# Kernel optimization log

Hardware: AMD Instinct MI355X
Metric: run time of the kernel (lower is better)

## Reference

```python
import jax, jax.numpy as jnp
import numpy as np

B, S, D = 2, 2048, 1024
H, HD = 16, 64  # num_heads, head_dim; H*HD == D


def setup_inputs() -> dict:
    key = jax.random.key(0)
    ks = jax.random.split(key, 5)
    scale = 1.0 / np.sqrt(D)
    return {
        "inputs": jax.random.normal(ks[0], (B, S, D), jnp.float32),
        "Wq": jax.random.normal(ks[1], (D, H * HD), jnp.float32) * scale,
        "bq": jnp.zeros((H * HD,), jnp.float32),
        "Wk": jax.random.normal(ks[2], (D, H * HD), jnp.float32) * scale,
        "bk": jnp.zeros((H * HD,), jnp.float32),
        "Wv": jax.random.normal(ks[3], (D, H * HD), jnp.float32) * scale,
        "bv": jnp.zeros((H * HD,), jnp.float32),
        "Wo": jax.random.normal(ks[4], (H * HD, D), jnp.float32) * scale,
        "bo": jnp.zeros((D,), jnp.float32),
    }


def reference(inputs, Wq, bq, Wk, bk, Wv, bv, Wo, bo):
    b, s, _ = inputs.shape
    # QKV projections, split into heads: [b, s, H, HD]
    q = (inputs @ Wq + bq).reshape(b, s, H, HD)
    k = (inputs @ Wk + bk).reshape(b, s, H, HD)
    v = (inputs @ Wv + bv).reshape(b, s, H, HD)
    # scaled dot-product attention (non-causal, full)
    scores = jnp.einsum('bqhd,bkhd->bhqk', q, k) / jnp.sqrt(jnp.float32(HD))
    attn = jax.nn.softmax(scores, axis=-1)
    out = jnp.einsum('bhql,blhd->bqhd', attn, v).reshape(b, s, H * HD)
    return out @ Wo + bo
```

## Files before the change

### kernel.cpp

```cpp
#include <hip/hip_runtime.h>
#include <hip/hip_bf16.h>

typedef __attribute__((ext_vector_type(8))) _Float16 half8;
typedef __attribute__((ext_vector_type(4))) _Float16 half4;
typedef __attribute__((ext_vector_type(2))) _Float16 half2v;
typedef __attribute__((ext_vector_type(4))) __fp16 fp16x4;
typedef __attribute__((ext_vector_type(4))) float f32x4;

#define MFMA16(a, b, c) __builtin_amdgcn_mfma_f32_16x16x32_f16(a, b, c, 0, 0, 0)
#define MFMA16K16(a, b, c)                                                         \
    __builtin_amdgcn_mfma_f32_16x16x16f16(__builtin_bit_cast(fp16x4, a),           \
                                          __builtin_bit_cast(fp16x4, b), c, 0, 0, 0)

typedef const __attribute__((address_space(1))) unsigned int GU32;
typedef __attribute__((address_space(3))) unsigned int LU32;

__device__ __forceinline__ void async_copy16(const _Float16* g, _Float16* l) {
    __builtin_amdgcn_global_load_lds((GU32*)g, (LU32*)l, 16, 0, 0);
}

__device__ __forceinline__ half2v pack2(float a, float b) {
    return __builtin_bit_cast(half2v, __builtin_amdgcn_cvt_pkrtz(a, b));
}

#define QSCALE 0.18033688011112042f


__global__ __launch_bounds__(256) void prep(
    const float* __restrict__ X, _Float16* __restrict__ Xh,
    const float* __restrict__ W0, const float* __restrict__ W1,
    const float* __restrict__ W2, const float* __restrict__ W3,
    _Float16* __restrict__ T0, _Float16* __restrict__ T1,
    _Float16* __restrict__ T2, _Float16* __restrict__ T3) {
    __shared__ float t[32][33];
    const int bid = blockIdx.x, tid = threadIdx.x;
    if (bid < 4096) {
        int i = (bid * 256 + tid) * 4;
        float4 v = *(const float4*)(X + i);
        half4 o = {(_Float16)v.x, (_Float16)v.y, (_Float16)v.z, (_Float16)v.w};
        *(half4*)(Xh + i) = o;
    } else {
        const int bid2 = bid - 4096;
        const int z = bid2 >> 10, tt = bid2 & 1023;
        const int bx = tt & 31, by = tt >> 5;
        const int tx = tid & 31, ty = tid >> 5;
        const float* src = z == 0 ? W0 : z == 1 ? W1 : z == 2 ? W2 : W3;
        _Float16* dst    = z == 0 ? T0 : z == 1 ? T1 : z == 2 ? T2 : T3;
        const int x = bx * 32 + tx;
        const int y0 = by * 32;
        for (int i = ty; i < 32; i += 8)
            t[i][tx] = src[(size_t)(y0 + i) * 1024 + x];
        __syncthreads();
        const int nx = y0 + tx;
        const int ny = bx * 32;
        for (int i = ty; i < 32; i += 8)
            dst[(size_t)(ny + i) * 1024 + nx] = (_Float16)t[tx][i];
    }
}

__global__ __launch_bounds__(256) void qkv_gemm(
    const _Float16* __restrict__ Xh,
    const _Float16* __restrict__ WTq, const _Float16* __restrict__ WTk,
    const _Float16* __restrict__ WTv,
    const float* __restrict__ bq, const float* __restrict__ bk,
    const float* __restrict__ bv,
    _Float16* __restrict__ Qo, _Float16* __restrict__ Ko,
    _Float16* __restrict__ Vto) {
    __shared__ __attribute__((aligned(16))) _Float16 Als[128 * 32];
    __shared__ __attribute__((aligned(16))) _Float16 Bls[128 * 32];

    const int wsel = blockIdx.y >> 3;
    const _Float16* WT = wsel == 0 ? WTq : wsel == 1 ? WTk : WTv;
    const float* bias  = wsel == 0 ? bq  : wsel == 1 ? bk  : bv;

    const int tid = threadIdx.x, w = tid >> 6, lane = tid & 63;
    const int quad = lane >> 4, l16 = lane & 15;
    const int wr = (w >> 1) * 64, wc = (w & 1) * 64;
    const int mBase = blockIdx.x * 128, nBase = (blockIdx.y & 7) * 128;
    const _Float16* Ab = Xh + (size_t)mBase * 1024;
    const _Float16* Bb = WT + (size_t)nBase * 1024;

    const int sr0 = tid >> 2,          sc0 = (tid & 3) ^ ((sr0 >> 1) & 3);
    const int sr1 = (256 + tid) >> 2,  sc1 = (tid & 3) ^ ((sr1 >> 1) & 3);

    f32x4 acc[4][4] = {};

    for (int k0 = 0; k0 < 1024; k0 += 32) {
        __syncthreads();
        {
            _Float16* lA0 = Als + (size_t)(tid & 192) * 8;
            _Float16* lB0 = Bls + (size_t)(tid & 192) * 8;
            _Float16* lA1 = Als + (size_t)(256 + (tid & 192)) * 8;
            _Float16* lB1 = Bls + (size_t)(256 + (tid & 192)) * 8;
            async_copy16(Ab + (size_t)sr0 * 1024 + k0 + sc0 * 8, lA0);
            async_copy16(Bb + (size_t)sr0 * 1024 + k0 + sc0 * 8, lB0);
            async_copy16(Ab + (size_t)sr1 * 1024 + k0 + sc1 * 8, lA1);
            async_copy16(Bb + (size_t)sr1 * 1024 + k0 + sc1 * 8, lB1);
        }
        __syncthreads();
        half8 af[4], bfr[4];
#pragma unroll
        for (int i = 0; i < 4; ++i) {
            const int row = wr + i * 16 + l16;
            af[i] = ((const half8*)Als)[row * 4 + (quad ^ ((row >> 1) & 3))];
        }
#pragma unroll
        for (int j = 0; j < 4; ++j) {
            const int row = wc + j * 16 + l16;
            bfr[j] = ((const half8*)Bls)[row * 4 + (quad ^ ((row >> 1) & 3))];
        }
#pragma unroll
        for (int i = 0; i < 4; ++i)
#pragma unroll
            for (int j = 0; j < 4; ++j) acc[i][j] = MFMA16(af[i], bfr[j], acc[i][j]);
    }

    const float scale = (wsel == 0) ? QSCALE : 1.0f;
#pragma unroll
    for (int i = 0; i < 4; ++i) {
        const int row = mBase + wr + i * 16 + quad * 4;
#pragma unroll
        for (int j = 0; j < 4; ++j) {
            const int col = nBase + wc + j * 16 + l16;
            const float bb = bias[col];
            if (wsel == 2) {
                const int hh = col >> 6, hd = col & 63;
                const int bi = row >> 11, s = row & 2047;
                half4 pv;
#pragma unroll
                for (int r = 0; r < 4; ++r) pv[r] = (_Float16)((acc[i][j][r] + bb) * scale);
                *(half4*)(Vto + ((size_t)(bi * 16 + hh) * 64 + hd) * 2048 + s) = pv;
            } else {
                _Float16* dst = (wsel == 0) ? Qo : Ko;
#pragma unroll
                for (int r = 0; r < 4; ++r)
                    dst[(size_t)(row + r) * 1024 + col] =
                        (_Float16)((acc[i][j][r] + bb) * scale);
            }
        }
    }
}

__global__ __launch_bounds__(512) void attn_kernel(
    const _Float16* __restrict__ Q, const _Float16* __restrict__ K,
    const _Float16* __restrict__ Vt, _Float16* __restrict__ O) {
    const int bh = blockIdx.y;
    const int b = bh >> 4, h = bh & 15;
    const int qt = blockIdx.x;
    const int tid = threadIdx.x, w = tid >> 6, lane = tid & 63;
    const int quad = lane >> 4, l16 = lane & 15;
    const int ws2 = w & 3, kstream = w >> 2;

    __shared__ __attribute__((aligned(16))) _Float16 smem[32768];
    _Float16 (*Kls)[2][4096] = (_Float16(*)[2][4096])smem;
    _Float16 (*Vls)[2][4096] = (_Float16(*)[2][4096])(smem + 16384);

    const _Float16* Qb = Q  + (size_t)b * 2048 * 1024 + h * 64;
    const _Float16* Kb = K  + (size_t)b * 2048 * 1024 + h * 64;
    const _Float16* Vb = Vt + (size_t)bh * 64 * 2048;

    const int stid = tid & 255, sgrp = tid >> 8;
    const int u0 = stid, u1 = 256 + stid;
    const int r0 = u0 >> 3, c0 = (u0 & 7) ^ (r0 & 7);
    const int r1 = u1 >> 3, c1 = (u1 & 7) ^ (r1 & 7);
    const int lbase0 = (stid & 192) * 8;
    const int lbase1 = 2048 + (stid & 192) * 8;

    half8 qf[2][2];
#pragma unroll
    for (int g = 0; g < 2; ++g) {
        const int q = qt * 128 + ws2 * 32 + g * 16 + l16;
#pragma unroll
        for (int kc = 0; kc < 2; ++kc)
            qf[g][kc] = *(const half8*)(Qb + (size_t)q * 1024 + kc * 32 + quad * 8);
    }

    f32x4 oacc[2][4] = {};
    float l[2] = {0.f, 0.f};

    {
        const int nb = sgrp * 64;
        _Float16* kd = &Kls[sgrp][0][0];
        _Float16* vd = &Vls[sgrp][0][0];
        async_copy16(Kb + (size_t)(nb + r0) * 1024 + c0 * 8, kd + lbase0);
        async_copy16(Kb + (size_t)(nb + r1) * 1024 + c1 * 8, kd + lbase1);
        async_copy16(Vb + (size_t)r0 * 2048 + nb + c0 * 8, vd + lbase0);
        async_copy16(Vb + (size_t)r1 * 2048 + nb + c1 * 8, vd + lbase1);
    }

    const int sw = l16 & 7;
    for (int it = 0; it < 16; ++it) {
        __syncthreads();
        const _Float16* Kc = &Kls[kstream][it & 1][0];
        const _Float16* Vc = &Vls[kstream][it & 1][0];
        if (it + 1 < 16) {
            const int nb = (2 * (it + 1) + sgrp) * 64;
            _Float16* kd = &Kls[sgrp][(it + 1) & 1][0];
            _Float16* vd = &Vls[sgrp][(it + 1) & 1][0];
            async_copy16(Kb + (size_t)(nb + r0) * 1024 + c0 * 8, kd + lbase0);
            async_copy16(Kb + (size_t)(nb + r1) * 1024 + c1 * 8, kd + lbase1);
            async_copy16(Vb + (size_t)r0 * 2048 + nb + c0 * 8, vd + lbase0);
            async_copy16(Vb + (size_t)r1 * 2048 + nb + c1 * 8, vd + lbase1);
        }
        f32x4 s0[4] = {}, s1[4] = {};
#pragma unroll
        for (int nt = 0; nt < 4; ++nt) {
            const int key = nt * 16 + l16;
            half8 k0 = *(const half8*)(Kc + ((size_t)key * 8 + (quad ^ sw)) * 8);
            half8 k1 = *(const half8*)(Kc + ((size_t)key * 8 + ((4 + quad) ^ sw)) * 8);
            s0[nt] = MFMA16(k0, qf[0][0], s0[nt]);
            s0[nt] = MFMA16(k1, qf[0][1], s0[nt]);
            s1[nt] = MFMA16(k0, qf[1][0], s1[nt]);
            s1[nt] = MFMA16(k1, qf[1][1], s1[nt]);
        }
        half4 pB[2][4];
#pragma unroll
        for (int g = 0; g < 2; ++g) {
            f32x4* s = g ? s1 : s0;
#pragma unroll
            for (int nt = 0; nt < 4; ++nt) {
                float p0 = __builtin_amdgcn_exp2f(s[nt][0]);
                float p1 = __builtin_amdgcn_exp2f(s[nt][1]);
                float p2 = __builtin_amdgcn_exp2f(s[nt][2]);
                float p3 = __builtin_amdgcn_exp2f(s[nt][3]);
                l[g] += (p0 + p1) + (p2 + p3);
                ((half2v*)&pB[g][nt])[0] = pack2(p0, p1);
                ((half2v*)&pB[g][nt])[1] = pack2(p2, p3);
            }
        }
#pragma unroll
        for (int nt = 0; nt < 4; ++nt) {
            const int chunk = (nt << 1) + (quad >> 1);
#pragma unroll
            for (int j = 0; j < 4; ++j) {
                const int hd = j * 16 + l16;
                half4 vf = *(const half4*)(Vc + ((size_t)hd * 8 + (chunk ^ sw)) * 8 +
                                           (quad & 1) * 4);
                oacc[0][j] = MFMA16K16(vf, pB[0][nt], oacc[0][j]);
                oacc[1][j] = MFMA16K16(vf, pB[1][nt], oacc[1][j]);
            }
        }
    }
    __syncthreads();
    float* red  = (float*)smem;
    float* redl = (float*)smem + 4 * 64 * 36;
    const int rb = (ws2 * 64 + lane) * 36;
    if (kstream == 1) {
#pragma unroll
        for (int g = 0; g < 2; ++g) {
#pragma unroll
            for (int j = 0; j < 4; ++j)
                *(f32x4*)&red[rb + (g * 4 + j) * 4] = oacc[g][j];
            redl[(ws2 * 64 + lane) * 2 + g] = l[g];
        }
    }
    __syncthreads();
    if (kstream == 0) {
#pragma unroll
        for (int g = 0; g < 2; ++g) {
#pragma unroll
            for (int j = 0; j < 4; ++j) {
                f32x4 o2 = *(const f32x4*)&red[rb + (g * 4 + j) * 4];
#pragma unroll
                for (int r = 0; r < 4; ++r) oacc[g][j][r] += o2[r];
            }
            float lt = l[g] + redl[(ws2 * 64 + lane) * 2 + g];
            lt += __shfl_xor(lt, 16);
            lt += __shfl_xor(lt, 32);
            const float inv = __builtin_amdgcn_rcpf(lt);
            const int token = b * 2048 + qt * 128 + ws2 * 32 + g * 16 + l16;
#pragma unroll
            for (int j = 0; j < 4; ++j) {
                half4 ov;
#pragma unroll
                for (int r = 0; r < 4; ++r) ov[r] = (_Float16)(oacc[g][j][r] * inv);
                *(half4*)&O[(size_t)token * 1024 + h * 64 + j * 16 + quad * 4] = ov;
            }
        }
    }
}

__global__ __launch_bounds__(256) void out_gemm(
    const _Float16* __restrict__ Oh, const _Float16* __restrict__ WTo,
    const float* __restrict__ bo, float* __restrict__ Y) {
    __shared__ __attribute__((aligned(16))) _Float16 Als[64 * 32];
    __shared__ __attribute__((aligned(16))) _Float16 Bls[128 * 32];
    const int tid = threadIdx.x, w = tid >> 6, lane = tid & 63;
    const int quad = lane >> 4, l16 = lane & 15;
    const int wr = (w >> 1) * 32, wc = (w & 1) * 64;
    const int mBase = blockIdx.x * 64, nBase = blockIdx.y * 128;
    const _Float16* Ab = Oh + (size_t)mBase * 1024;
    const _Float16* Bb = WTo + (size_t)nBase * 1024;

    const int sr0 = tid >> 2,         sc0 = (tid & 3) ^ ((sr0 >> 1) & 3);
    const int sr1 = (256 + tid) >> 2, sc1 = (tid & 3) ^ ((sr1 >> 1) & 3);

    f32x4 acc[2][4] = {};
    for (int k0 = 0; k0 < 1024; k0 += 32) {
        __syncthreads();
        {
            _Float16* lA0 = Als + (size_t)(tid & 192) * 8;
            _Float16* lB0 = Bls + (size_t)(tid & 192) * 8;
            _Float16* lB1 = Bls + (size_t)(256 + (tid & 192)) * 8;
            async_copy16(Ab + (size_t)sr0 * 1024 + k0 + sc0 * 8, lA0);
            async_copy16(Bb + (size_t)sr0 * 1024 + k0 + sc0 * 8, lB0);
            async_copy16(Bb + (size_t)sr1 * 1024 + k0 + sc1 * 8, lB1);
        }
        __syncthreads();
        half8 af[2], bfr[4];
#pragma unroll
        for (int i = 0; i < 2; ++i) {
            const int row = wr + i * 16 + l16;
            af[i] = ((const half8*)Als)[row * 4 + (quad ^ ((row >> 1) & 3))];
        }
#pragma unroll
        for (int j = 0; j < 4; ++j) {
            const int row = wc + j * 16 + l16;
            bfr[j] = ((const half8*)Bls)[row * 4 + (quad ^ ((row >> 1) & 3))];
        }
#pragma unroll
        for (int i = 0; i < 2; ++i)
#pragma unroll
            for (int j = 0; j < 4; ++j) acc[i][j] = MFMA16(af[i], bfr[j], acc[i][j]);
    }
#pragma unroll
    for (int i = 0; i < 2; ++i) {
        const int row = mBase + wr + i * 16 + quad * 4;
#pragma unroll
        for (int j = 0; j < 4; ++j) {
            const int col = nBase + wc + j * 16 + l16;
            const float bb = bo[col];
#pragma unroll
            for (int r = 0; r < 4; ++r)
                Y[(size_t)(row + r) * 1024 + col] = acc[i][j][r] + bb;
        }
    }
}

extern "C" void kernel_launch(void* const* d_in, const int* in_sizes, int n_in,
                              void* d_out, int out_size, void* d_ws, size_t ws_size,
                              hipStream_t stream) {
    const float* X  = (const float*)d_in[0];
    const float* Wq = (const float*)d_in[1];
    const float* bq = (const float*)d_in[2];
    const float* Wk = (const float*)d_in[3];
    const float* bk = (const float*)d_in[4];
    const float* Wv = (const float*)d_in[5];
    const float* bv = (const float*)d_in[6];
    const float* Wo = (const float*)d_in[7];
    const float* bo = (const float*)d_in[8];
    float* Y = (float*)d_out;

    char* ws = (char*)d_ws;
    _Float16* Xh  = (_Float16*)(ws);
    _Float16* WTq = (_Float16*)(ws + (8ull << 20));
    _Float16* WTk = (_Float16*)(ws + (10ull << 20));
    _Float16* WTv = (_Float16*)(ws + (12ull << 20));
    _Float16* WTo = (_Float16*)(ws + (14ull << 20));
    _Float16* Qh  = (_Float16*)(ws + (16ull << 20));
    _Float16* Kh  = (_Float16*)(ws + (24ull << 20));
    _Float16* Vth = (_Float16*)(ws + (32ull << 20));
    _Float16* Oh  = (_Float16*)(ws + (40ull << 20));

    prep<<<8192, 256, 0, stream>>>(X, Xh, Wq, Wk, Wv, Wo, WTq, WTk, WTv, WTo);
    qkv_gemm<<<dim3(32, 24), 256, 0, stream>>>(Xh, WTq, WTk, WTv, bq, bk, bv, Qh, Kh, Vth);
    attn_kernel<<<dim3(16, 32), 512, 0, stream>>>(Qh, Kh, Vth, Oh);
    out_gemm<<<dim3(64, 8), 256, 0, stream>>>(Oh, WTo, bo, Y);
}
```

Baseline: 199.4 us.

## Double-buffer LDS tiles in QKV and output projection GEMMs

Both projection GEMMs now keep two LDS buffers per operand. Each iteration issues the async global-to-LDS copy for the next K tile before running the MFMAs on the current tile, and one barrier per iteration replaces two. This lets global load latency overlap with matrix math instead of stalling every step. The cost is twice the shared memory per block, which may reduce occupancy.

Result: no change. 195.9 us (-1.8%).

```diff
diff --git a/kernel.cpp b/kernel.cpp
--- a/kernel.cpp
+++ b/kernel.cpp
@@ -66,8 +66,8 @@
     const float* __restrict__ bv,
     _Float16* __restrict__ Qo, _Float16* __restrict__ Ko,
     _Float16* __restrict__ Vto) {
-    __shared__ __attribute__((aligned(16))) _Float16 Als[128 * 32];
-    __shared__ __attribute__((aligned(16))) _Float16 Bls[128 * 32];
+    __shared__ __attribute__((aligned(16))) _Float16 Als[2][128 * 32];
+    __shared__ __attribute__((aligned(16))) _Float16 Bls[2][128 * 32];
 
     const int wsel = blockIdx.y >> 3;
     const _Float16* WT = wsel == 0 ? WTq : wsel == 1 ? WTk : WTv;
@@ -82,32 +82,39 @@
 
     const int sr0 = tid >> 2,          sc0 = (tid & 3) ^ ((sr0 >> 1) & 3);
     const int sr1 = (256 + tid) >> 2,  sc1 = (tid & 3) ^ ((sr1 >> 1) & 3);
+    const int lb0 = (tid & 192) * 8;
+    const int lb1 = (256 + (tid & 192)) * 8;
+
+    async_copy16(Ab + (size_t)sr0 * 1024 + sc0 * 8, &Als[0][0] + lb0);
+    async_copy16(Bb + (size_t)sr0 * 1024 + sc0 * 8, &Bls[0][0] + lb0);
+    async_copy16(Ab + (size_t)sr1 * 1024 + sc1 * 8, &Als[0][0] + lb1);
+    async_copy16(Bb + (size_t)sr1 * 1024 + sc1 * 8, &Bls[0][0] + lb1);
 
     f32x4 acc[4][4] = {};
 
-    for (int k0 = 0; k0 < 1024; k0 += 32) {
+    for (int it = 0; it < 32; ++it) {
         __syncthreads();
-        {
-            _Float16* lA0 = Als + (size_t)(tid & 192) * 8;
-            _Float16* lB0 = Bls + (size_t)(tid & 192) * 8;
-            _Float16* lA1 = Als + (size_t)(256 + (tid & 192)) * 8;
-            _Float16* lB1 = Bls + (size_t)(256 + (tid & 192)) * 8;
-            async_copy16(Ab + (size_t)sr0 * 1024 + k0 + sc0 * 8, lA0);
-            async_copy16(Bb + (size_t)sr0 * 1024 + k0 + sc0 * 8, lB0);
-            async_copy16(Ab + (size_t)sr1 * 1024 + k0 + sc1 * 8, lA1);
-            async_copy16(Bb + (size_t)sr1 * 1024 + k0 + sc1 * 8, lB1);
-        }
-        __syncthreads();
+        const _Float16* Ac = &Als[it & 1][0];
+        const _Float16* Bc = &Bls[it & 1][0];
+        if (it + 1 < 32) {
+            const int k1 = (it + 1) * 32;
+            _Float16* Ad = &Als[(it + 1) & 1][0];
+            _Float16* Bd = &Bls[(it + 1) & 1][0];
+            async_copy16(Ab + (size_t)sr0 * 1024 + k1 + sc0 * 8, Ad + lb0);
+            async_copy16(Bb + (size_t)sr0 * 1024 + k1 + sc0 * 8, Bd + lb0);
+            async_copy16(Ab + (size_t)sr1 * 1024 + k1 + sc1 * 8, Ad + lb1);
+            async_copy16(Bb + (size_t)sr1 * 1024 + k1 + sc1 * 8, Bd + lb1);
+        }
         half8 af[4], bfr[4];
 #pragma unroll
         for (int i = 0; i < 4; ++i) {
             const int row = wr + i * 16 + l16;
-            af[i] = ((const half8*)Als)[row * 4 + (quad ^ ((row >> 1) & 3))];
+            af[i] = ((const half8*)Ac)[row * 4 + (quad ^ ((row >> 1) & 3))];
         }
 #pragma unroll
         for (int j = 0; j < 4; ++j) {
             const int row = wc + j * 16 + l16;
-            bfr[j] = ((const half8*)Bls)[row * 4 + (quad ^ ((row >> 1) & 3))];
+            bfr[j] = ((const half8*)Bc)[row * 4 + (quad ^ ((row >> 1) & 3))];
         }
 #pragma unroll
         for (int i = 0; i < 4; ++i)
@@ -283,8 +290,8 @@
 __global__ __launch_bounds__(256) void out_gemm(
     const _Float16* __restrict__ Oh, const _Float16* __restrict__ WTo,
     const float* __restrict__ bo, float* __restrict__ Y) {
-    __shared__ __attribute__((aligned(16))) _Float16 Als[64 * 32];
-    __shared__ __attribute__((aligned(16))) _Float16 Bls[128 * 32];
+    __shared__ __attribute__((aligned(16))) _Float16 Als[2][64 * 32];
+    __shared__ __attribute__((aligned(16))) _Float16 Bls[2][128 * 32];
     const int tid = threadIdx.x, w = tid >> 6, lane = tid & 63;
     const int quad = lane >> 4, l16 = lane & 15;
     const int wr = (w >> 1) * 32, wc = (w & 1) * 64;
@@ -294,29 +301,36 @@
 
     const int sr0 = tid >> 2,         sc0 = (tid & 3) ^ ((sr0 >> 1) & 3);
     const int sr1 = (256 + tid) >> 2, sc1 = (tid & 3) ^ ((sr1 >> 1) & 3);
+    const int lb0 = (tid & 192) * 8;
+    const int lb1 = (256 + (tid & 192)) * 8;
+
+    async_copy16(Ab + (size_t)sr0 * 1024 + sc0 * 8, &Als[0][0] + lb0);
+    async_copy16(Bb + (size_t)sr0 * 1024 + sc0 * 8, &Bls[0][0] + lb0);
+    async_copy16(Bb + (size_t)sr1 * 1024 + sc1 * 8, &Bls[0][0] + lb1);
 
     f32x4 acc[2][4] = {};
-    for (int k0 = 0; k0 < 1024; k0 += 32) {
+    for (int it = 0; it < 32; ++it) {
         __syncthreads();
-        {
-            _Float16* lA0 = Als + (size_t)(tid & 192) * 8;
-            _Float16* lB0 = Bls + (size_t)(tid & 192) * 8;
-            _Float16* lB1 = Bls + (size_t)(256 + (tid & 192)) * 8;
-            async_copy16(Ab + (size_t)sr0 * 1024 + k0 + sc0 * 8, lA0);
-            async_copy16(Bb + (size_t)sr0 * 1024 + k0 + sc0 * 8, lB0);
-            async_copy16(Bb + (size_t)sr1 * 1024 + k0 + sc1 * 8, lB1);
-        }
-        __syncthreads();
+        const _Float16* Ac = &Als[it & 1][0];
+        const _Float16* Bc = &Bls[it & 1][0];
+        if (it + 1 < 32) {
+            const int k1 = (it + 1) * 32;
+            _Float16* Ad = &Als[(it + 1) & 1][0];
+            _Float16* Bd = &Bls[(it + 1) & 1][0];
+            async_copy16(Ab + (size_t)sr0 * 1024 + k1 + sc0 * 8, Ad + lb0);
+            async_copy16(Bb + (size_t)sr0 * 1024 + k1 + sc0 * 8, Bd + lb0);
+            async_copy16(Bb + (size_t)sr1 * 1024 + k1 + sc1 * 8, Bd + lb1);
+        }
         half8 af[2], bfr[4];
 #pragma unroll
         for (int i = 0; i < 2; ++i) {
             const int row = wr + i * 16 + l16;
-            af[i] = ((const half8*)Als)[row * 4 + (quad ^ ((row >> 1) & 3))];
+            af[i] = ((const half8*)Ac)[row * 4 + (quad ^ ((row >> 1) & 3))];
         }
 #pragma unroll
         for (int j = 0; j < 4; ++j) {
             const int row = wc + j * 16 + l16;
-            bfr[j] = ((const half8*)Bls)[row * 4 + (quad ^ ((row >> 1) & 3))];
+            bfr[j] = ((const half8*)Bc)[row * 4 + (quad ^ ((row >> 1) & 3))];
         }
 #pragma unroll
         for (int i = 0; i < 2; ++i)
```
